# Optimization experiments

Measured on AMD Instinct MI355X. Metric: run time of the kernel, lower is better.

Reference implementation:

```python
import jax, jax.numpy as jnp
import numpy as np

B, T, D = 4, 2048, 1024
H = 16
HD = D // H  # 64
SCALE = 1.0 / np.sqrt(HD).astype(np.float32)


def setup_inputs() -> dict:
    key = jax.random.key(0)
    ks = jax.random.split(key, 5)
    std = 0.02
    return {
        "x": jax.random.normal(ks[0], (B, T, D), dtype=jnp.float32),
        "wq": jax.random.normal(ks[1], (D, D), dtype=jnp.float32) * std,
        "wk": jax.random.normal(ks[2], (D, D), dtype=jnp.float32) * std,
        "wv": jax.random.normal(ks[3], (D, D), dtype=jnp.float32) * std,
        "wo": jax.random.normal(ks[4], (D, D), dtype=jnp.float32) * std,
    }


def _shape(t):
    # [B,T,D] -> [B,H,T,HD]
    Bt, Tt, _ = t.shape
    return t.reshape(Bt, Tt, H, HD).transpose(0, 2, 1, 3)


def reference(x, wq, wk, wv, wo):
    # Linear layers are y = x @ W^T (torch nn.Linear semantics, no bias)
    q = _shape(x @ wq.T)  # [B,H,T,HD]
    k = _shape(x @ wk.T)
    v = _shape(x @ wv.T)
    att = jnp.einsum("bhqd,bhkd->bhqk", q, k) * SCALE  # [B,H,T,T]
    # causal mask: -inf strictly above diagonal
    causal = jnp.triu(jnp.full((T, T), -jnp.inf, dtype=att.dtype), k=1)
    att = att + causal[None, None, :, :]
    att = jax.nn.softmax(att.astype(jnp.float32), axis=-1).astype(att.dtype)
    # dropout prob = 0.0 -> identity
    y = jnp.einsum("bhqk,bhkd->bhqd", att, v)  # [B,H,T,HD]
    y = y.transpose(0, 2, 1, 3).reshape(B, T, D)
    return y @ wo.T
```

## Files before the change

### kernel.cpp

```cpp
#include <hip/hip_runtime.h>
#include <hip/hip_bf16.h>

#define BB 4
#define TT 2048
#define DDIM 1024
#define HH 16
#define HD 64

typedef __bf16 bf16_t;
typedef __bf16 bf16x4 __attribute__((ext_vector_type(4)));
typedef __bf16 bf16x8 __attribute__((ext_vector_type(8)));
typedef float f32x4 __attribute__((ext_vector_type(4)));

#define GLOAD_LDS(gp, lp) \
    __builtin_amdgcn_global_load_lds( \
        (const __attribute__((address_space(1))) void*)(gp), \
        (__attribute__((address_space(3))) void*)(lp), 16, 0, 0)

__global__ __launch_bounds__(256) void cvt_f32_bf16(
    const float* __restrict__ src, bf16_t* __restrict__ dst, size_t n8)
{
    size_t i = (size_t)blockIdx.x * blockDim.x + threadIdx.x;
    const size_t stride = (size_t)gridDim.x * blockDim.x;
    for (; i < n8; i += stride) {
        const f32x4 a = ((const f32x4*)src)[2 * i];
        const f32x4 b = ((const f32x4*)src)[2 * i + 1];
        bf16x8 v;
#pragma unroll
        for (int j = 0; j < 4; j++) { v[j] = (bf16_t)a[j]; v[4 + j] = (bf16_t)b[j]; }
        ((bf16x8*)dst)[i] = v;
    }
}

__global__ __launch_bounds__(256) void cvt_wpack(
    const float* __restrict__ s0, const float* __restrict__ s1,
    const float* __restrict__ s2, const float* __restrict__ s3,
    bf16_t* __restrict__ dst)
{
    const size_t n8 = (size_t)4 * DDIM * DDIM / 8;
    size_t i = (size_t)blockIdx.x * blockDim.x + threadIdx.x;
    const size_t stride = (size_t)gridDim.x * blockDim.x;
    for (; i < n8; i += stride) {
        const int sel = (int)(i >> 17);
        const float* s = sel == 0 ? s0 : sel == 1 ? s1 : sel == 2 ? s2 : s3;
        const size_t off8 = i & ((1u << 17) - 1);
        const f32x4 a = ((const f32x4*)s)[2 * off8];
        const f32x4 b = ((const f32x4*)s)[2 * off8 + 1];
        bf16x8 v;
#pragma unroll
        for (int j = 0; j < 4; j++) { v[j] = (bf16_t)a[j]; v[4 + j] = (bf16_t)b[j]; }
        ((bf16x8*)dst)[i] = v;
    }
}

__device__ __forceinline__ void stage8(const bf16_t* __restrict__ g, int ld,
                                       bf16_t* __restrict__ ldsbase, int lane)
{
    const int rr = lane >> 3;
    const int cc = (lane & 7) ^ ((rr & 1) << 2);
    GLOAD_LDS(&g[(size_t)rr * ld + cc * 8], ldsbase);
}

__global__ __launch_bounds__(256) void gemm_qkv(
    const bf16_t* __restrict__ A, const bf16_t* __restrict__ Wqkv,
    bf16_t* __restrict__ Qo, bf16_t* __restrict__ Ko, bf16_t* __restrict__ Vto,
    int M, int K)
{
    __shared__ alignas(16) bf16_t As[128 * 64];
    __shared__ alignas(16) bf16_t Bs[128 * 64];

    const int tid  = threadIdx.x;
    const int lane = tid & 63;
    const int w    = tid >> 6;
    const int quad = lane >> 4;
    const int l15  = lane & 15;
    const int wm   = (w >> 1) * 64;
    const int wn   = (w & 1) * 64;
    const int tileN = blockIdx.x * 128;
    const int tileM = blockIdx.y * 128;

    const f32x4 vzero = {0.f, 0.f, 0.f, 0.f};
    f32x4 acc[4][4];
#pragma unroll
    for (int i = 0; i < 4; i++)
#pragma unroll
        for (int j = 0; j < 4; j++) acc[i][j] = vzero;

    const int par4 = (l15 & 1) << 2;

    for (int k0 = 0; k0 < K; k0 += 64) {
        __syncthreads();
#pragma unroll
        for (int q = 0; q < 4; q++) {
            const int r0 = w * 32 + q * 8;
            stage8(&A[(size_t)(tileM + r0) * K + k0], K, &As[r0 * 64], lane);
            stage8(&Wqkv[(size_t)(tileN + r0) * K + k0], K, &Bs[r0 * 64], lane);
        }
        __syncthreads();

#pragma unroll
        for (int ss = 0; ss < 2; ss++) {
            const int phys = ((ss * 4 + quad) ^ par4) << 3;
            bf16x8 af[4], bf[4];
#pragma unroll
            for (int i = 0; i < 4; i++)
                af[i] = *(bf16x8*)&As[(wm + i * 16 + l15) * 64 + phys];
#pragma unroll
            for (int j = 0; j < 4; j++)
                bf[j] = *(bf16x8*)&Bs[(wn + j * 16 + l15) * 64 + phys];
#pragma unroll
            for (int i = 0; i < 4; i++)
#pragma unroll
                for (int j = 0; j < 4; j++)
                    acc[i][j] = __builtin_amdgcn_mfma_f32_16x16x32_bf16(
                        af[i], bf[j], acc[i][j], 0, 0, 0);
        }
    }

    const int region = tileN >> 10;
#pragma unroll
    for (int i = 0; i < 4; i++) {
        const int row = tileM + wm + i * 16 + quad * 4;
#pragma unroll
        for (int j = 0; j < 4; j++) {
            const int ncol = tileN + wn + j * 16 + l15;
            if (region == 2) {
                const int cl = ncol - 2048;
                const int h = cl >> 6, d = cl & 63;
                const int bb = row >> 11, tloc = row & (TT - 1);
                bf16x4 pk;
#pragma unroll
                for (int r = 0; r < 4; r++) pk[r] = (bf16_t)acc[i][j][r];
                *(bf16x4*)&Vto[(((size_t)bb * HH + h) * HD + d) * TT + tloc] = pk;
            } else {
                bf16_t* dst = (region == 0) ? Qo : Ko;
                const int cl = ncol & 1023;
#pragma unroll
                for (int r = 0; r < 4; r++)
                    dst[(size_t)(row + r) * DDIM + cl] = (bf16_t)acc[i][j][r];
            }
        }
    }
}

__global__ __launch_bounds__(256) void gemm_out(
    const bf16_t* __restrict__ A, const bf16_t* __restrict__ Bm,
    float* __restrict__ C, int M, int N, int K)
{
    __shared__ alignas(16) bf16_t As[64 * 64];
    __shared__ alignas(16) bf16_t Bs[128 * 64];

    const int tid  = threadIdx.x;
    const int lane = tid & 63;
    const int w    = tid >> 6;
    const int quad = lane >> 4;
    const int l15  = lane & 15;
    const int wm   = (w >> 1) * 32;
    const int wn   = (w & 1) * 64;
    const int tileN = blockIdx.x * 128;
    const int tileM = blockIdx.y * 64;

    const f32x4 vzero = {0.f, 0.f, 0.f, 0.f};
    f32x4 acc[2][4];
#pragma unroll
    for (int i = 0; i < 2; i++)
#pragma unroll
        for (int j = 0; j < 4; j++) acc[i][j] = vzero;

    const int par4 = (l15 & 1) << 2;

    for (int k0 = 0; k0 < K; k0 += 64) {
        __syncthreads();
#pragma unroll
        for (int q = 0; q < 2; q++) {
            const int r0 = w * 16 + q * 8;
            stage8(&A[(size_t)(tileM + r0) * K + k0], K, &As[r0 * 64], lane);
        }
#pragma unroll
        for (int q = 0; q < 4; q++) {
            const int r0 = w * 32 + q * 8;
            stage8(&Bm[(size_t)(tileN + r0) * K + k0], K, &Bs[r0 * 64], lane);
        }
        __syncthreads();

#pragma unroll
        for (int ss = 0; ss < 2; ss++) {
            const int phys = ((ss * 4 + quad) ^ par4) << 3;
            bf16x8 af[2], bf[4];
#pragma unroll
            for (int i = 0; i < 2; i++)
                af[i] = *(bf16x8*)&As[(wm + i * 16 + l15) * 64 + phys];
#pragma unroll
            for (int j = 0; j < 4; j++)
                bf[j] = *(bf16x8*)&Bs[(wn + j * 16 + l15) * 64 + phys];
#pragma unroll
            for (int i = 0; i < 2; i++)
#pragma unroll
                for (int j = 0; j < 4; j++)
                    acc[i][j] = __builtin_amdgcn_mfma_f32_16x16x32_bf16(
                        af[i], bf[j], acc[i][j], 0, 0, 0);
        }
    }

#pragma unroll
    for (int i = 0; i < 2; i++) {
#pragma unroll
        for (int r = 0; r < 4; r++) {
            const int row = tileM + wm + i * 16 + quad * 4 + r;
#pragma unroll
            for (int j = 0; j < 4; j++)
                C[(size_t)row * N + tileN + wn + j * 16 + l15] = acc[i][j][r];
        }
    }
}

__global__ __launch_bounds__(256, 2) void attn_causal(
    const bf16_t* __restrict__ Q, const bf16_t* __restrict__ Kg,
    const bf16_t* __restrict__ Vt_g, bf16_t* __restrict__ Y)
{
    __shared__ alignas(16) bf16_t Ks[64 * 72];
    __shared__ alignas(16) bf16_t Vt[64 * 72];
    __shared__ alignas(16) bf16_t Ps[4][32 * 72];

    const int tid  = threadIdx.x;
    const int lane = tid & 63;
    const int w    = tid >> 6;
    const int quad = lane >> 4;
    const int l15  = lane & 15;
    const int bh   = blockIdx.x;
    const int sp   = blockIdx.y;
    const int b = bh >> 4, h = bh & 15;

    const int stg_row = tid >> 3;
    const int stg_c8  = (tid & 7) * 8;

    const f32x4 vzero = {0.f, 0.f, 0.f, 0.f};
    bf16x8 ones;
#pragma unroll
    for (int j = 0; j < 8; j++) ones[j] = (l15 == 0) ? (bf16_t)1.0f : (bf16_t)0.0f;

    const bf16_t* kg0 = &Kg[(size_t)(b * TT + stg_row) * DDIM + h * 64 + stg_c8];
    const bf16_t* vg0 = &Vt_g[((size_t)bh * HD + stg_row) * TT + stg_c8];
    bf16_t* ksd = &Ks[stg_row * 72 + stg_c8];
    bf16_t* vtd = &Vt[stg_row * 72 + stg_c8];

    const float SC_LOG2E = 0.125f * 1.44269504f;

#pragma unroll 1
    for (int half = 0; half < 2; half++) {
        const int strip = half ? (15 - sp) : sp;
        const int qbase = strip * 128;

        bf16x8 qf[2][2];
#pragma unroll
        for (int mi = 0; mi < 2; mi++) {
            const size_t rq =
                (size_t)(b * TT + qbase + w * 32 + mi * 16 + l15) * DDIM + h * 64;
            qf[mi][0] = *(const bf16x8*)&Q[rq + quad * 8];
            qf[mi][1] = *(const bf16x8*)&Q[rq + 32 + quad * 8];
        }

        f32x4 o[2][4], o4[2];
#pragma unroll
        for (int mi = 0; mi < 2; mi++) {
#pragma unroll
            for (int c = 0; c < 4; c++) o[mi][c] = vzero;
            o4[mi] = vzero;
        }

        const int nkt = 2 * strip + 2;

        bf16x8 kreg[2], vreg[2];
#pragma unroll
        for (int p = 0; p < 2; p++) {
            kreg[p] = *(const bf16x8*)&kg0[(size_t)(p * 32) * DDIM];
            vreg[p] = *(const bf16x8*)&vg0[(size_t)(p * 32) * TT];
        }

#pragma unroll 1
        for (int kt = 0; kt < nkt; kt++) {
            const int kbase = kt * 64;
            __syncthreads();
#pragma unroll
            for (int p = 0; p < 2; p++) {
                *(bf16x8*)&ksd[p * 32 * 72] = kreg[p];
                *(bf16x8*)&vtd[p * 32 * 72] = vreg[p];
            }
            if (kt + 1 < nkt) {
                const int nb = (kt + 1) * 64;
#pragma unroll
                for (int p = 0; p < 2; p++) {
                    kreg[p] = *(const bf16x8*)&kg0[(size_t)(nb + p * 32) * DDIM];
                    vreg[p] = *(const bf16x8*)&vg0[(size_t)(p * 32) * TT + nb];
                }
            }
            __syncthreads();

            f32x4 s[2][4];
            __builtin_amdgcn_s_setprio(1);
#pragma unroll
            for (int c = 0; c < 4; c++) {
                bf16x8 kf0 = *(bf16x8*)&Ks[(c * 16 + l15) * 72 + quad * 8];
                bf16x8 kf1 = *(bf16x8*)&Ks[(c * 16 + l15) * 72 + 32 + quad * 8];
#pragma unroll
                for (int mi = 0; mi < 2; mi++) {
                    f32x4 t = __builtin_amdgcn_mfma_f32_16x16x32_bf16(
                        qf[mi][0], kf0, vzero, 0, 0, 0);
                    s[mi][c] = __builtin_amdgcn_mfma_f32_16x16x32_bf16(
                        qf[mi][1], kf1, t, 0, 0, 0);
                }
            }
            __builtin_amdgcn_s_setprio(0);

#pragma unroll
            for (int mi = 0; mi < 2; mi++) {
                const int qlow = qbase + w * 32 + mi * 16;
                const bool need = (kbase + 63 > qlow);
#pragma unroll
                for (int r = 0; r < 4; r++) {
                    const int qrow = qlow + quad * 4 + r;
                    const int prow = mi * 16 + quad * 4 + r;
#pragma unroll
                    for (int c = 0; c < 4; c++) {
                        float sv = s[mi][c][r] * SC_LOG2E;
                        if (need && (kbase + c * 16 + l15 > qrow)) sv = -1e30f;
                        const int pchunk = (c * 2 + (l15 >> 3)) ^ (prow >> 2);
                        Ps[w][prow * 72 + (pchunk << 3) + (l15 & 7)] =
                            (bf16_t)__builtin_amdgcn_exp2f(sv);
                    }
                }
            }

            __builtin_amdgcn_s_setprio(1);
#pragma unroll
            for (int ss = 0; ss < 2; ss++) {
                bf16x8 pf[2];
#pragma unroll
                for (int mi = 0; mi < 2; mi++) {
                    const int m = mi * 16 + l15;
                    pf[mi] = *(bf16x8*)&Ps[w][m * 72 +
                                              ((((ss * 4 + quad) ^ (m >> 2)) & 7) << 3)];
                }
#pragma unroll
                for (int c = 0; c < 4; c++) {
                    bf16x8 vf = *(bf16x8*)&Vt[(c * 16 + l15) * 72 + ss * 32 + quad * 8];
#pragma unroll
                    for (int mi = 0; mi < 2; mi++)
                        o[mi][c] = __builtin_amdgcn_mfma_f32_16x16x32_bf16(
                            pf[mi], vf, o[mi][c], 0, 0, 0);
                }
#pragma unroll
                for (int mi = 0; mi < 2; mi++)
                    o4[mi] = __builtin_amdgcn_mfma_f32_16x16x32_bf16(
                        pf[mi], ones, o4[mi], 0, 0, 0);
            }
            __builtin_amdgcn_s_setprio(0);
        }

#pragma unroll
        for (int mi = 0; mi < 2; mi++) {
#pragma unroll
            for (int r = 0; r < 4; r++) {
                const float lsum = __shfl(o4[mi][r], lane & 48, 64);
                const float inv = 1.0f / lsum;
                const int q = qbase + w * 32 + mi * 16 + quad * 4 + r;
#pragma unroll
                for (int c = 0; c < 4; c++)
                    Y[(size_t)(b * TT + q) * DDIM + h * 64 + c * 16 + l15] =
                        (bf16_t)(o[mi][c][r] * inv);
            }
        }
    }
}

extern "C" void kernel_launch(void* const* d_in, const int* in_sizes, int n_in,
                              void* d_out, int out_size, void* d_ws, size_t ws_size,
                              hipStream_t stream) {
    (void)in_sizes; (void)n_in; (void)out_size;
    const float* x  = (const float*)d_in[0];
    float* out = (float*)d_out;

    const int M = BB * TT;
    const size_t REGION = (size_t)M * DDIM;
    const size_t WREG   = (size_t)DDIM * DDIM;
    const size_t BATCH  = (size_t)TT * DDIM;
    bf16_t* ws = (bf16_t*)d_ws;

    if (ws_size >= (72ull << 20)) {
        bf16_t* xb  = ws;
        bf16_t* wpk = ws + REGION;
        bf16_t* Qb  = wpk + 4 * WREG;
        bf16_t* Kb  = Qb + REGION;
        bf16_t* Vtb = Kb + REGION;

        cvt_f32_bf16<<<1024, 256, 0, stream>>>(x, xb, REGION / 8);
        cvt_wpack<<<512, 256, 0, stream>>>(
            (const float*)d_in[1], (const float*)d_in[2],
            (const float*)d_in[3], (const float*)d_in[4], wpk);

        gemm_qkv<<<dim3(24, M / 128), 256, 0, stream>>>(
            xb, wpk, Qb, Kb, Vtb, M, DDIM);
        attn_causal<<<dim3(BB * HH, 8), 256, 0, stream>>>(Qb, Kb, Vtb, Qb);
        gemm_out<<<dim3(8, M / 64), 256, 0, stream>>>(
            Qb, wpk + 3 * WREG, out, M, DDIM, DDIM);
    } else {
        bf16_t* wpk = ws;
        bf16_t* xbb = ws + 4 * WREG;
        bf16_t* Qb  = xbb + BATCH;
        bf16_t* Kb  = Qb + BATCH;
        bf16_t* Vtb = Kb + BATCH;

        cvt_wpack<<<512, 256, 0, stream>>>(
            (const float*)d_in[1], (const float*)d_in[2],
            (const float*)d_in[3], (const float*)d_in[4], wpk);

        for (int b = 0; b < BB; b++) {
            const float* x_b = x + (size_t)b * BATCH;
            float* out_b = out + (size_t)b * BATCH;
            cvt_f32_bf16<<<512, 256, 0, stream>>>(x_b, xbb, BATCH / 8);
            gemm_qkv<<<dim3(24, TT / 128), 256, 0, stream>>>(
                xbb, wpk, Qb, Kb, Vtb, TT, DDIM);
            attn_causal<<<dim3(HH, 8), 256, 0, stream>>>(Qb, Kb, Vtb, Qb);
            gemm_out<<<dim3(8, TT / 64), 256, 0, stream>>>(
                Qb, wpk + 3 * WREG, out_b, TT, DDIM, DDIM);
        }
    }
}
```

Before: 258.4 us.

## Double-buffer QKV GEMM with larger 256x192 tiles and 512-thread blocks

The QKV projection GEMM now uses 256x192 block tiles across 8 waves and double-buffered LDS. The next K-slice is prefetched with global_load_lds while the current slice is consumed. MFMA bursts are wrapped in s_setprio and separated by intra-iteration barriers to interleave waves. This aims to hide global load latency and raise data reuse per tile, at the cost of more LDS (112KB per block) and register pressure, plus fewer blocks in the grid (16x32).

```diff
diff --git a/kernel.cpp b/kernel.cpp
--- a/kernel.cpp
+++ b/kernel.cpp
@@ -61,69 +61,96 @@
     GLOAD_LDS(&g[(size_t)rr * ld + cc * 8], ldsbase);
 }
 
-__global__ __launch_bounds__(256) void gemm_qkv(
+__global__ __launch_bounds__(512, 2) void gemm_qkv(
     const bf16_t* __restrict__ A, const bf16_t* __restrict__ Wqkv,
     bf16_t* __restrict__ Qo, bf16_t* __restrict__ Ko, bf16_t* __restrict__ Vto,
     int M, int K)
 {
-    __shared__ alignas(16) bf16_t As[128 * 64];
-    __shared__ alignas(16) bf16_t Bs[128 * 64];
+    __shared__ alignas(16) bf16_t As[2][256 * 64];
+    __shared__ alignas(16) bf16_t Bs[2][192 * 64];
 
     const int tid  = threadIdx.x;
     const int lane = tid & 63;
     const int w    = tid >> 6;
     const int quad = lane >> 4;
     const int l15  = lane & 15;
-    const int wm   = (w >> 1) * 64;
-    const int wn   = (w & 1) * 64;
-    const int tileN = blockIdx.x * 128;
-    const int tileM = blockIdx.y * 128;
+    const int wm   = (w >> 2) * 128;
+    const int wn   = (w & 3) * 48;
+    const int tileN = blockIdx.x * 192;
+    const int tileM = blockIdx.y * 256;
 
     const f32x4 vzero = {0.f, 0.f, 0.f, 0.f};
-    f32x4 acc[4][4];
-#pragma unroll
-    for (int i = 0; i < 4; i++)
-#pragma unroll
-        for (int j = 0; j < 4; j++) acc[i][j] = vzero;
+    f32x4 acc[8][3];
+#pragma unroll
+    for (int i = 0; i < 8; i++)
+#pragma unroll
+        for (int j = 0; j < 3; j++) acc[i][j] = vzero;
 
     const int par4 = (l15 & 1) << 2;
 
-    for (int k0 = 0; k0 < K; k0 += 64) {
+#pragma unroll
+    for (int q = 0; q < 4; q++) {
+        const int r0 = w * 32 + q * 8;
+        stage8(&A[(size_t)(tileM + r0) * K], K, &As[0][r0 * 64], lane);
+    }
+#pragma unroll
+    for (int q = 0; q < 3; q++) {
+        const int r0 = w * 24 + q * 8;
+        stage8(&Wqkv[(size_t)(tileN + r0) * K], K, &Bs[0][r0 * 64], lane);
+    }
+    __syncthreads();
+
+    const int NT = K >> 6;
+    for (int t = 0; t < NT; ++t) {
+        const int cur = t & 1;
+        if (t + 1 < NT) {
+            const int k0 = (t + 1) << 6;
+#pragma unroll
+            for (int q = 0; q < 4; q++) {
+                const int r0 = w * 32 + q * 8;
+                stage8(&A[(size_t)(tileM + r0) * K + k0], K,
+                       &As[cur ^ 1][r0 * 64], lane);
+            }
+#pragma unroll
+            for (int q = 0; q < 3; q++) {
+                const int r0 = w * 24 + q * 8;
+                stage8(&Wqkv[(size_t)(tileN + r0) * K + k0], K,
+                       &Bs[cur ^ 1][r0 * 64], lane);
+            }
+        }
+
+#pragma unroll
+        for (int p = 0; p < 4; ++p) {
+            const int mh = p & 1;
+            const int ss = p >> 1;
+            const int phys = ((ss * 4 + quad) ^ par4) << 3;
+            bf16x8 af[4], bfr[3];
+#pragma unroll
+            for (int i = 0; i < 4; i++)
+                af[i] = *(bf16x8*)&As[cur][(wm + (mh * 4 + i) * 16 + l15) * 64 + phys];
+#pragma unroll
+            for (int j = 0; j < 3; j++)
+                bfr[j] = *(bf16x8*)&Bs[cur][(wn + j * 16 + l15) * 64 + phys];
+            __builtin_amdgcn_s_setprio(1);
+#pragma unroll
+            for (int i = 0; i < 4; i++)
+#pragma unroll
+                for (int j = 0; j < 3; j++)
+                    acc[mh * 4 + i][j] = __builtin_amdgcn_mfma_f32_16x16x32_bf16(
+                        af[i], bfr[j], acc[mh * 4 + i][j], 0, 0, 0);
+            __builtin_amdgcn_s_setprio(0);
+            if (p < 3) __builtin_amdgcn_s_barrier();
+        }
         __syncthreads();
-#pragma unroll
-        for (int q = 0; q < 4; q++) {
-            const int r0 = w * 32 + q * 8;
-            stage8(&A[(size_t)(tileM + r0) * K + k0], K, &As[r0 * 64], lane);
-            stage8(&Wqkv[(size_t)(tileN + r0) * K + k0], K, &Bs[r0 * 64], lane);
-        }
-        __syncthreads();
-
-#pragma unroll
-        for (int ss = 0; ss < 2; ss++) {
-            const int phys = ((ss * 4 + quad) ^ par4) << 3;
-            bf16x8 af[4], bf[4];
-#pragma unroll
-            for (int i = 0; i < 4; i++)
-                af[i] = *(bf16x8*)&As[(wm + i * 16 + l15) * 64 + phys];
-#pragma unroll
-            for (int j = 0; j < 4; j++)
-                bf[j] = *(bf16x8*)&Bs[(wn + j * 16 + l15) * 64 + phys];
-#pragma unroll
-            for (int i = 0; i < 4; i++)
-#pragma unroll
-                for (int j = 0; j < 4; j++)
-                    acc[i][j] = __builtin_amdgcn_mfma_f32_16x16x32_bf16(
-                        af[i], bf[j], acc[i][j], 0, 0, 0);
-        }
-    }
-
-    const int region = tileN >> 10;
-#pragma unroll
-    for (int i = 0; i < 4; i++) {
+    }
+
+#pragma unroll
+    for (int i = 0; i < 8; i++) {
         const int row = tileM + wm + i * 16 + quad * 4;
 #pragma unroll
-        for (int j = 0; j < 4; j++) {
+        for (int j = 0; j < 3; j++) {
             const int ncol = tileN + wn + j * 16 + l15;
+            const int region = ncol >> 10;
             if (region == 2) {
                 const int cl = ncol - 2048;
                 const int h = cl >> 6, d = cl & 63;
@@ -398,7 +425,7 @@
             (const float*)d_in[1], (const float*)d_in[2],
             (const float*)d_in[3], (const float*)d_in[4], wpk);
 
-        gemm_qkv<<<dim3(24, M / 128), 256, 0, stream>>>(
+        gemm_qkv<<<dim3(16, M / 256), 512, 0, stream>>>(
             xb, wpk, Qb, Kb, Vtb, M, DDIM);
         attn_causal<<<dim3(BB * HH, 8), 256, 0, stream>>>(Qb, Kb, Vtb, Qb);
         gemm_out<<<dim3(8, M / 64), 256, 0, stream>>>(
@@ -418,7 +445,7 @@
             const float* x_b = x + (size_t)b * BATCH;
             float* out_b = out + (size_t)b * BATCH;
             cvt_f32_bf16<<<512, 256, 0, stream>>>(x_b, xbb, BATCH / 8);
-            gemm_qkv<<<dim3(24, TT / 128), 256, 0, stream>>>(
+            gemm_qkv<<<dim3(16, TT / 256), 512, 0, stream>>>(
                 xbb, wpk, Qb, Kb, Vtb, TT, DDIM);
             attn_causal<<<dim3(HH, 8), 256, 0, stream>>>(Qb, Kb, Vtb, Qb);
             gemm_out<<<dim3(8, TT / 64), 256, 0, stream>>>(
```

After: 295.5 us. +14.4%, slower.
